# Optimization experiments

Hardware: AMD Instinct MI355X
Metric: run time of the kernel (lower is better)

## Reference

```python
import jax, jax.numpy as jnp
import numpy as np

B, S, D, H = 2, 2048, 2048, 16
NEG = -1e9


def setup_inputs() -> dict:
    key = jax.random.key(0)
    ks = jax.random.split(key, 5)
    x = jax.random.normal(ks[0], (B, S, D), dtype=jnp.float32)
    # additive causal mask: 0 on/below diagonal, -1e9 above
    causal = jnp.triu(jnp.full((S, S), NEG, dtype=jnp.float32), k=1)
    attn_mask = causal[None, None, :, :]  # [1,1,S,S]
    scale = 0.02
    Wq = jax.random.normal(ks[1], (D, D), dtype=jnp.float32) * scale
    Wk = jax.random.normal(ks[2], (D, D), dtype=jnp.float32) * scale
    Wv = jax.random.normal(ks[3], (D, D), dtype=jnp.float32) * scale
    Wo = jax.random.normal(ks[4], (D, D), dtype=jnp.float32) * scale
    return {"x": x, "attn_mask": attn_mask, "Wq": Wq, "Wk": Wk, "Wv": Wv, "Wo": Wo}


def reference(x, attn_mask, Wq, Wk, Wv, Wo):
    b, s, hidden = x.shape
    d = hidden // H
    # torch nn.Linear: y = x @ W.T (no bias since bias=None)
    q = (x @ Wq.T).reshape(b, s, H, d).transpose(0, 2, 1, 3)  # [b,h,s,d]
    k = (x @ Wk.T).reshape(b, s, H, d).transpose(0, 2, 1, 3)
    v = (x @ Wv.T).reshape(b, s, H, d).transpose(0, 2, 1, 3)
    q = q * (1.0 / float(d) ** 0.5)
    att = jnp.einsum("bhqd,bhkd->bhqk", q, k) + attn_mask  # [b,h,s,s]
    att = jax.nn.softmax(att.astype(jnp.float32), axis=-1).astype(x.dtype)
    y = jnp.einsum("bhqk,bhkd->bhqd", att, v)
    y = y.transpose(0, 2, 1, 3).reshape(b, s, hidden)
    return y @ Wo.T
```

## Files before the change

### kernel.cpp

```cpp
#include <hip/hip_runtime.h>
#include <hip/hip_bf16.h>
#include <cstdint>
#include <cstddef>

typedef __bf16 bf16;
typedef __bf16 bf16x8 __attribute__((ext_vector_type(8)));
typedef __bf16 bf16x4 __attribute__((ext_vector_type(4)));
typedef float f32x4 __attribute__((ext_vector_type(4)));

static constexpr int BATCH = 2;
static constexpr int SEQ = 2048;
static constexpr int DMODEL = 2048;
static constexpr int NH = 16;
static constexpr int HD = 128;
static constexpr int MROWS = BATCH * SEQ;

#define GLOBAL_AS(p) ((const __attribute__((address_space(1))) void*)(p))
#define LDS_AS(p)    ((__attribute__((address_space(3))) void*)(p))

__global__ void cvt_kernel(const float* __restrict__ src, bf16* __restrict__ dst, int n4) {
  int i = blockIdx.x * blockDim.x + threadIdx.x;
  if (i < n4) {
    float4 f = reinterpret_cast<const float4*>(src)[i];
    bf16x4 o;
    o.x = (bf16)f.x; o.y = (bf16)f.y; o.z = (bf16)f.z; o.w = (bf16)f.w;
    reinterpret_cast<bf16x4*>(dst)[i] = o;
  }
}

enum { MODE_QKV = 0, MODE_OUT = 1 };

template <int MODE>
__global__ __launch_bounds__(256, 2) void gemm_bt(
    const bf16* __restrict__ A, const bf16* __restrict__ W,
    bf16* __restrict__ Oq, bf16* __restrict__ Ok, bf16* __restrict__ Ov,
    float* __restrict__ Oout) {
  constexpr int Kd = DMODEL;
  __shared__ __align__(16) bf16 As[128][64];
  __shared__ __align__(16) bf16 Bs[128][64];
  const int n0 = blockIdx.x * 128;
  const int m0 = blockIdx.y * 128;
  const int tid = threadIdx.x;
  const int wave = tid >> 6;
  const int lane = tid & 63;
  const int quad = lane >> 4;
  const int l16 = lane & 15;
  const int wm = (wave >> 1) * 64;
  const int wn = (wave & 1) * 64;
  const int sr = lane >> 3;
  const int sc = (lane & 7) * 8;

  f32x4 acc[4][4] = {};
  for (int kt = 0; kt < Kd; kt += 64) {
#pragma unroll
    for (int i = 0; i < 4; i++) {
      const int r = wave * 32 + i * 8;
      __builtin_amdgcn_global_load_lds(
          GLOBAL_AS(&A[(size_t)(m0 + r + sr) * Kd + kt + sc]), LDS_AS(&As[r][0]), 16, 0, 0);
      __builtin_amdgcn_global_load_lds(
          GLOBAL_AS(&W[(size_t)(n0 + r + sr) * Kd + kt + sc]), LDS_AS(&Bs[r][0]), 16, 0, 0);
    }
    __syncthreads();
#pragma unroll
    for (int ks = 0; ks < 2; ks++) {
      bf16x8 af[4], bfr[4];
#pragma unroll
      for (int t = 0; t < 4; t++)
        af[t] = *reinterpret_cast<const bf16x8*>(&As[wm + t * 16 + l16][ks * 32 + quad * 8]);
#pragma unroll
      for (int t = 0; t < 4; t++)
        bfr[t] = *reinterpret_cast<const bf16x8*>(&Bs[wn + t * 16 + l16][ks * 32 + quad * 8]);
#pragma unroll
      for (int tm = 0; tm < 4; tm++)
#pragma unroll
        for (int tn = 0; tn < 4; tn++)
          acc[tm][tn] = __builtin_amdgcn_mfma_f32_16x16x32_bf16(af[tm], bfr[tn], acc[tm][tn], 0, 0, 0);
    }
    __syncthreads();
  }
#pragma unroll
  for (int tm = 0; tm < 4; tm++) {
#pragma unroll
    for (int tn = 0; tn < 4; tn++) {
      const int row0 = m0 + wm + tm * 16 + quad * 4;
      if constexpr (MODE == MODE_OUT) {
        const int col = n0 + wn + tn * 16 + l16;
#pragma unroll
        for (int j = 0; j < 4; j++)
          Oout[(size_t)(row0 + j) * DMODEL + col] = acc[tm][tn][j];
      } else {
        const int mat = n0 >> 11;
        const int col = (n0 & 2047) + wn + tn * 16 + l16;
        const int h = col >> 7, dd = col & 127;
        if (mat == 2) {
          const int b = row0 >> 11, s = row0 & 2047;
          bf16x4 pk;
#pragma unroll
          for (int j = 0; j < 4; j++) pk[j] = (bf16)acc[tm][tn][j];
          *reinterpret_cast<bf16x4*>(&Ov[((size_t)(b * NH + h) * HD + dd) * SEQ + s]) = pk;
        } else {
          bf16* O = mat ? Ok : Oq;
          const float scale = mat ? 1.0f : 0.08838834764831845f;
#pragma unroll
          for (int j = 0; j < 4; j++) {
            const int row = row0 + j;
            const int b = row >> 11, s = row & 2047;
            O[((size_t)(b * NH + h) * SEQ + s) * HD + dd] = (bf16)(acc[tm][tn][j] * scale);
          }
        }
      }
    }
  }
}

__global__ __launch_bounds__(256, 2) void attn_kernel(
    const bf16* __restrict__ Q, const bf16* __restrict__ K,
    const bf16* __restrict__ Vt, bf16* __restrict__ Y) {
  const int j = blockIdx.x;
  const int bh = blockIdx.y;
  __shared__ __align__(16) char smem[54528];
  auto Ks  = (bf16(*)[128])smem;
  auto Vts = (bf16(*)[64])(smem + 16384);
  auto Ps  = (bf16(*)[16][72])(smem + 32768);
  const int tid = threadIdx.x;
  const int wave = tid >> 6;
  const int lane = tid & 63;
  const int quad = lane >> 4;
  const int l16 = lane & 15;

  const bf16* Kbh = K + (size_t)bh * SEQ * HD;
  const bf16* Vbh = Vt + (size_t)bh * HD * SEQ;
  const int b = bh >> 4, h = bh & 15;

  const int krow = lane >> 4;
  const int vrow = lane >> 3;
  const int vchunk = ((lane & 7) - vrow) & 7;

  for (int pass = 0; pass < 2; ++pass) {
    const int qt = pass ? (31 - j) : j;
    const int q0 = qt * 64;
    const int ntiles = qt + 1;

    const bf16* Qw = Q + ((size_t)bh * SEQ + q0 + wave * 16) * HD;
    bf16x8 qf[4];
#pragma unroll
    for (int kk = 0; kk < 4; kk++)
      qf[kk] = *reinterpret_cast<const bf16x8*>(&Qw[(size_t)l16 * HD + kk * 32 + quad * 8]);

    f32x4 oacc[8] = {};
    float m_i = -3.0e38f, l_i = 0.f;

    for (int t = 0; t < ntiles; ++t) {
      const int kt = t * 64;
#pragma unroll
      for (int i = 0; i < 4; i++) {
        const int rbase = wave * 16 + i * 4;
        const int r = rbase + krow;
        const int c = ((lane & 15) - krow - i * 4) & 15;
        __builtin_amdgcn_global_load_lds(
            GLOBAL_AS(&Kbh[(size_t)(kt + r) * HD + c * 8]), LDS_AS(&Ks[rbase][0]), 16, 0, 0);
      }
#pragma unroll
      for (int i = 0; i < 4; i++) {
        const int rbase = wave * 32 + i * 8;
        const int r = rbase + vrow;
        __builtin_amdgcn_global_load_lds(
            GLOBAL_AS(&Vbh[(size_t)r * SEQ + kt + vchunk * 8]), LDS_AS(&Vts[rbase][0]), 16, 0, 0);
      }
      __syncthreads();

      f32x4 sacc[4] = {};
#pragma unroll
      for (int kk = 0; kk < 4; kk++) {
        const int kcol = (((kk * 4 + quad + l16) & 15)) * 8;
        bf16x8 ka[4];
#pragma unroll
        for (int mt = 0; mt < 4; mt++)
          ka[mt] = *reinterpret_cast<const bf16x8*>(&Ks[mt * 16 + l16][kcol]);
#pragma unroll
        for (int mt = 0; mt < 4; mt++)
          sacc[mt] = __builtin_amdgcn_mfma_f32_16x16x32_bf16(ka[mt], qf[kk], sacc[mt], 0, 0, 0);
      }

      const int qg_loc = wave * 16 + l16;
      float mx = -3.0e38f;
      if (t == ntiles - 1) {
#pragma unroll
        for (int mt = 0; mt < 4; mt++)
#pragma unroll
          for (int jj = 0; jj < 4; jj++) {
            const int kg = mt * 16 + quad * 4 + jj;
            float v = (kg <= qg_loc) ? sacc[mt][jj] : -3.0e38f;
            sacc[mt][jj] = v;
            mx = fmaxf(mx, v);
          }
      } else {
#pragma unroll
        for (int mt = 0; mt < 4; mt++)
#pragma unroll
          for (int jj = 0; jj < 4; jj++) mx = fmaxf(mx, sacc[mt][jj]);
      }
      mx = fmaxf(mx, __shfl_xor(mx, 16));
      mx = fmaxf(mx, __shfl_xor(mx, 32));
      const float mnew = fmaxf(m_i, mx);
      const float alpha = __expf(m_i - mnew);
      m_i = mnew;
      float rs = 0.f;
#pragma unroll
      for (int mt = 0; mt < 4; mt++)
#pragma unroll
        for (int jj = 0; jj < 4; jj++) {
          float p = __expf(sacc[mt][jj] - mnew);
          sacc[mt][jj] = p;
          rs += p;
        }
      rs += __shfl_xor(rs, 16);
      rs += __shfl_xor(rs, 32);
      l_i = l_i * alpha + rs;
#pragma unroll
      for (int mt8 = 0; mt8 < 8; mt8++)
#pragma unroll
        for (int jj = 0; jj < 4; jj++) oacc[mt8][jj] *= alpha;

#pragma unroll
      for (int mt = 0; mt < 4; mt++) {
        bf16x4 pk;
#pragma unroll
        for (int jj = 0; jj < 4; jj++) pk[jj] = (bf16)sacc[mt][jj];
        *reinterpret_cast<bf16x4*>(&Ps[wave][l16][mt * 16 + quad * 4]) = pk;
      }

#pragma unroll
      for (int kk2 = 0; kk2 < 2; kk2++) {
        const int vcol = ((kk2 * 4 + quad + l16) & 7) * 8;
        bf16x8 pb = *reinterpret_cast<const bf16x8*>(&Ps[wave][l16][kk2 * 32 + quad * 8]);
#pragma unroll
        for (int mt8 = 0; mt8 < 8; mt8++) {
          bf16x8 av = *reinterpret_cast<const bf16x8*>(&Vts[mt8 * 16 + l16][vcol]);
          oacc[mt8] = __builtin_amdgcn_mfma_f32_16x16x32_bf16(av, pb, oacc[mt8], 0, 0, 0);
        }
      }
      __syncthreads();
    }

    const float inv = 1.0f / l_i;
    const int qg = q0 + wave * 16 + l16;
#pragma unroll
    for (int mt8 = 0; mt8 < 8; mt8++) {
      bf16x4 pk;
#pragma unroll
      for (int jj = 0; jj < 4; jj++) pk[jj] = (bf16)(oacc[mt8][jj] * inv);
      *reinterpret_cast<bf16x4*>(
          &Y[(size_t)(b * SEQ + qg) * DMODEL + h * HD + mt8 * 16 + quad * 4]) = pk;
    }
  }
}

extern "C" void kernel_launch(void* const* d_in, const int* in_sizes, int n_in,
                              void* d_out, int out_size, void* d_ws, size_t ws_size,
                              hipStream_t stream) {
  const float* x  = (const float*)d_in[0];
  const float* Wq = (const float*)d_in[2];
  const float* Wk = (const float*)d_in[3];
  const float* Wv = (const float*)d_in[4];
  const float* Wo = (const float*)d_in[5];
  float* out = (float*)d_out;

  char* ws = (char*)d_ws;
  bf16* xb  = (bf16*)(ws + 0);
  bf16* Wqb = (bf16*)(ws + 16777216);
  bf16* Wkb = (bf16*)(ws + 25165824);
  bf16* Wvb = (bf16*)(ws + 33554432);
  bf16* Wob = (bf16*)(ws + 41943040);
  bf16* Qb  = (bf16*)(ws + 50331648);
  bf16* Kb  = (bf16*)(ws + 67108864);
  bf16* Vtb = (bf16*)(ws + 83886080);
  bf16* Yb  = xb;
  if (ws_size < 100663296) return;

  const int nx4 = MROWS * DMODEL / 4;
  const int nw4 = DMODEL * DMODEL / 4;
  cvt_kernel<<<nx4 / 256, 256, 0, stream>>>(x, xb, nx4);
  cvt_kernel<<<nw4 / 256, 256, 0, stream>>>(Wq, Wqb, nw4);
  cvt_kernel<<<nw4 / 256, 256, 0, stream>>>(Wk, Wkb, nw4);
  cvt_kernel<<<nw4 / 256, 256, 0, stream>>>(Wv, Wvb, nw4);
  cvt_kernel<<<nw4 / 256, 256, 0, stream>>>(Wo, Wob, nw4);

  gemm_bt<MODE_QKV><<<dim3(48, MROWS / 128), 256, 0, stream>>>(
      xb, Wqb, Qb, Kb, Vtb, nullptr);

  attn_kernel<<<dim3(16, BATCH * NH), 256, 0, stream>>>(Qb, Kb, Vtb, Yb);

  gemm_bt<MODE_OUT><<<dim3(16, MROWS / 128), 256, 0, stream>>>(
      Yb, Wob, nullptr, nullptr, nullptr, out);
}
```

Baseline: 396.8 us.

## Swizzle GEMM LDS tiles, merge conversion kernels, raise GEMM occupancy bound

Measured after the change: 362.4 us. -8.7%, faster.

```diff
diff --git a/kernel.cpp b/kernel.cpp
--- a/kernel.cpp
+++ b/kernel.cpp
@@ -18,20 +18,30 @@
 #define GLOBAL_AS(p) ((const __attribute__((address_space(1))) void*)(p))
 #define LDS_AS(p)    ((__attribute__((address_space(3))) void*)(p))
 
-__global__ void cvt_kernel(const float* __restrict__ src, bf16* __restrict__ dst, int n4) {
-  int i = blockIdx.x * blockDim.x + threadIdx.x;
-  if (i < n4) {
-    float4 f = reinterpret_cast<const float4*>(src)[i];
-    bf16x4 o;
-    o.x = (bf16)f.x; o.y = (bf16)f.y; o.z = (bf16)f.z; o.w = (bf16)f.w;
-    reinterpret_cast<bf16x4*>(dst)[i] = o;
+__global__ void cvt5_kernel(const float* __restrict__ x,
+                            const float* __restrict__ wq, const float* __restrict__ wk,
+                            const float* __restrict__ wv, const float* __restrict__ wo,
+                            bf16* __restrict__ dst) {
+  const int i = blockIdx.x * blockDim.x + threadIdx.x;
+  const float* src;
+  int local;
+  if (i < 2097152) { src = x; local = i; }
+  else {
+    const int r = i - 2097152;
+    const int w = r >> 20;
+    local = r & 1048575;
+    src = (w == 0) ? wq : (w == 1) ? wk : (w == 2) ? wv : wo;
   }
+  float4 f = reinterpret_cast<const float4*>(src)[local];
+  bf16x4 o;
+  o.x = (bf16)f.x; o.y = (bf16)f.y; o.z = (bf16)f.z; o.w = (bf16)f.w;
+  reinterpret_cast<bf16x4*>(dst)[i] = o;
 }
 
 enum { MODE_QKV = 0, MODE_OUT = 1 };
 
 template <int MODE>
-__global__ __launch_bounds__(256, 2) void gemm_bt(
+__global__ __launch_bounds__(256, 4) void gemm_bt(
     const bf16* __restrict__ A, const bf16* __restrict__ W,
     bf16* __restrict__ Oq, bf16* __restrict__ Ok, bf16* __restrict__ Ov,
     float* __restrict__ Oout) {
@@ -47,8 +57,8 @@
   const int l16 = lane & 15;
   const int wm = (wave >> 1) * 64;
   const int wn = (wave & 1) * 64;
-  const int sr = lane >> 3;
-  const int sc = (lane & 7) * 8;
+  const int srow = lane >> 3;
+  const int schunk = ((lane & 7) - srow) & 7;
 
   f32x4 acc[4][4] = {};
   for (int kt = 0; kt < Kd; kt += 64) {
@@ -56,20 +66,23 @@
     for (int i = 0; i < 4; i++) {
       const int r = wave * 32 + i * 8;
       __builtin_amdgcn_global_load_lds(
-          GLOBAL_AS(&A[(size_t)(m0 + r + sr) * Kd + kt + sc]), LDS_AS(&As[r][0]), 16, 0, 0);
+          GLOBAL_AS(&A[(size_t)(m0 + r + srow) * Kd + kt + schunk * 8]),
+          LDS_AS(&As[r][0]), 16, 0, 0);
       __builtin_amdgcn_global_load_lds(
-          GLOBAL_AS(&W[(size_t)(n0 + r + sr) * Kd + kt + sc]), LDS_AS(&Bs[r][0]), 16, 0, 0);
+          GLOBAL_AS(&W[(size_t)(n0 + r + srow) * Kd + kt + schunk * 8]),
+          LDS_AS(&Bs[r][0]), 16, 0, 0);
     }
     __syncthreads();
 #pragma unroll
     for (int ks = 0; ks < 2; ks++) {
+      const int col = (((ks * 4 + quad + l16) & 7)) * 8;
       bf16x8 af[4], bfr[4];
 #pragma unroll
       for (int t = 0; t < 4; t++)
-        af[t] = *reinterpret_cast<const bf16x8*>(&As[wm + t * 16 + l16][ks * 32 + quad * 8]);
+        af[t] = *reinterpret_cast<const bf16x8*>(&As[wm + t * 16 + l16][col]);
 #pragma unroll
       for (int t = 0; t < 4; t++)
-        bfr[t] = *reinterpret_cast<const bf16x8*>(&Bs[wn + t * 16 + l16][ks * 32 + quad * 8]);
+        bfr[t] = *reinterpret_cast<const bf16x8*>(&Bs[wn + t * 16 + l16][col]);
 #pragma unroll
       for (int tm = 0; tm < 4; tm++)
 #pragma unroll
@@ -269,8 +282,6 @@
   char* ws = (char*)d_ws;
   bf16* xb  = (bf16*)(ws + 0);
   bf16* Wqb = (bf16*)(ws + 16777216);
-  bf16* Wkb = (bf16*)(ws + 25165824);
-  bf16* Wvb = (bf16*)(ws + 33554432);
   bf16* Wob = (bf16*)(ws + 41943040);
   bf16* Qb  = (bf16*)(ws + 50331648);
   bf16* Kb  = (bf16*)(ws + 67108864);
@@ -278,13 +289,7 @@
   bf16* Yb  = xb;
   if (ws_size < 100663296) return;
 
-  const int nx4 = MROWS * DMODEL / 4;
-  const int nw4 = DMODEL * DMODEL / 4;
-  cvt_kernel<<<nx4 / 256, 256, 0, stream>>>(x, xb, nx4);
-  cvt_kernel<<<nw4 / 256, 256, 0, stream>>>(Wq, Wqb, nw4);
-  cvt_kernel<<<nw4 / 256, 256, 0, stream>>>(Wk, Wkb, nw4);
-  cvt_kernel<<<nw4 / 256, 256, 0, stream>>>(Wv, Wvb, nw4);
-  cvt_kernel<<<nw4 / 256, 256, 0, stream>>>(Wo, Wob, nw4);
+  cvt5_kernel<<<24576, 256, 0, stream>>>(x, Wq, Wk, Wv, Wo, xb);
 
   gemm_bt<MODE_QKV><<<dim3(48, MROWS / 128), 256, 0, stream>>>(
       xb, Wqb, Qb, Kb, Vtb, nullptr);
```
